# Optimization experiments

Measured on AMD Instinct MI355X. Metric: run time of the kernel, lower is better.

The kernel has to match this reference:

```python
import jax, jax.numpy as jnp
import numpy as np

DIM = 192
HEADS = 6
HSP = 8
WSP = 8
POS_DIM = (DIM // 4) // 4  # 12


def _ln(x, g, b, eps=1e-5):
    m = jnp.mean(x, -1, keepdims=True)
    v = jnp.mean((x - m) ** 2, -1, keepdims=True)
    return (x - m) / jnp.sqrt(v + eps) * g + b


def _rel_tables():
    # rpe_biases: ((2*HSP-1)*(2*WSP-1), 2) float coords of all relative offsets
    bh, bw = np.meshgrid(np.arange(1 - HSP, HSP), np.arange(1 - WSP, WSP), indexing='ij')
    biases = np.stack([bh, bw], -1).reshape(-1, 2).astype(np.float32)
    # relative_position_index: (N, N) int lookup into the bias table
    ch, cw = np.meshgrid(np.arange(HSP), np.arange(WSP), indexing='ij')
    coords = np.stack([ch, cw], 0).reshape(2, -1)  # (2, N)
    rel = coords[:, :, None] - coords[:, None, :]  # (2, N, N)
    idx = (rel[0] + HSP - 1) * (2 * WSP - 1) + (rel[1] + WSP - 1)
    return jnp.asarray(biases), jnp.asarray(idx.astype(np.int32))


def setup_inputs() -> dict:
    key = jax.random.key(0)
    ks = jax.random.split(key, 8)
    B, H, W = 2, 256, 256
    L = H * W
    def lin(k, i, o):
        return jax.random.normal(k, (i, o), jnp.float32) * 0.02
    return {
        'qkv': jax.random.normal(ks[0], (3, B, L, DIM), jnp.float32),
        'w_proj': lin(ks[1], 2, POS_DIM), 'b_proj': jnp.zeros((POS_DIM,), jnp.float32),
        'g1': jnp.ones((POS_DIM,), jnp.float32), 'be1': jnp.zeros((POS_DIM,), jnp.float32),
        'w1': lin(ks[2], POS_DIM, POS_DIM), 'b1': jnp.zeros((POS_DIM,), jnp.float32),
        'g2': jnp.ones((POS_DIM,), jnp.float32), 'be2': jnp.zeros((POS_DIM,), jnp.float32),
        'w2': lin(ks[3], POS_DIM, POS_DIM), 'b2': jnp.zeros((POS_DIM,), jnp.float32),
        'g3': jnp.ones((POS_DIM,), jnp.float32), 'be3': jnp.zeros((POS_DIM,), jnp.float32),
        'w3': lin(ks[4], POS_DIM, HEADS), 'b3': jnp.zeros((HEADS,), jnp.float32),
        'H': H, 'W': W,
    }


def reference(qkv, w_proj, b_proj, g1, be1, w1, b1, g2, be2, w2, b2, g3, be3, w3, b3, H, W):
    B, L, C = qkv.shape[1], qkv.shape[2], qkv.shape[3]
    hd = C // HEADS
    scale = float(hd) ** -0.5
    N = HSP * WSP

    def im2win(x):
        # (B, L, C) -> (B*nW, heads, N, hd)
        x = x.reshape(B, H // HSP, HSP, W // WSP, WSP, C)
        x = x.transpose(0, 1, 3, 2, 4, 5).reshape(-1, N, HEADS, hd)
        return x.transpose(0, 2, 1, 3)

    q = im2win(qkv[0]) * scale
    k = im2win(qkv[1])
    v = im2win(qkv[2])

    attn = jnp.einsum('whnd,whmd->whnm', q, k)  # (B*nW, heads, N, N)

    # dynamic relative position bias via MLP (DynamicPosBias, residual=False)
    biases, rel_idx = _rel_tables()
    p = biases @ w_proj + b_proj
    p = jax.nn.relu(_ln(p, g1, be1)) @ w1 + b1
    p = jax.nn.relu(_ln(p, g2, be2)) @ w2 + b2
    p = jax.nn.relu(_ln(p, g3, be3)) @ w3 + b3  # (n_rel, heads)
    rpb = p[rel_idx.reshape(-1)].reshape(N, N, HEADS).transpose(2, 0, 1)  # (heads, N, N)
    attn = attn + rpb[None]

    attn = jax.nn.softmax(attn, axis=-1)
    x = jnp.einsum('whnm,whmd->whnd', attn, v)  # (B*nW, heads, N, hd)
    x = x.transpose(0, 2, 1, 3).reshape(-1, N, C)

    # windows2img: (B*nW, N, C) -> (B, H, W, C)
    x = x.reshape(B, H // HSP, W // WSP, HSP, WSP, C)
    x = x.transpose(0, 1, 3, 2, 4, 5).reshape(B, H, W, C)
    return x
```

## Files before the change

### kernel.cpp

```cpp
#include <hip/hip_runtime.h>
#include <hip/hip_bf16.h>

#define NHEADS 6
#define HD 32
#define CDIM 192
#define NTOK 64
#define NREL 225
#define PDIM 12
#define IMG 256
#define NWIN 2048
#define SCALE 0.17677669529663687f
#define INV_SCALE 5.656854249492381f

typedef __attribute__((ext_vector_type(8))) short v8s;
typedef __attribute__((ext_vector_type(4))) float v4f;

#define KS2 200
#define VTS 72
#define PTS 72

__device__ __forceinline__ unsigned pkbf(float x, float y) {
    __hip_bfloat162 h = __float22bfloat162_rn(make_float2(x, y));
    union { __hip_bfloat162 h; unsigned u; } c; c.h = h;
    return c.u;
}

__device__ __forceinline__ void ln_relu12(const float* x, const float* g,
                                          const float* be, float* y) {
    float m = 0.f;
#pragma unroll
    for (int i = 0; i < PDIM; ++i) m += x[i];
    m *= (1.f / PDIM);
    float v = 0.f;
#pragma unroll
    for (int i = 0; i < PDIM; ++i) { float d = x[i] - m; v += d * d; }
    v *= (1.f / PDIM);
    float inv = rsqrtf(v + 1e-5f);
#pragma unroll
    for (int i = 0; i < PDIM; ++i) {
        float t = (x[i] - m) * inv * g[i] + be[i];
        y[i] = t > 0.f ? t : 0.f;
    }
}

__global__ __launch_bounds__(512) void win_attn_fused(
    const float* __restrict__ qkv,
    const float* __restrict__ wp, const float* __restrict__ bp,
    const float* __restrict__ g1, const float* __restrict__ be1,
    const float* __restrict__ w1, const float* __restrict__ b1,
    const float* __restrict__ g2, const float* __restrict__ be2,
    const float* __restrict__ w2, const float* __restrict__ b2,
    const float* __restrict__ g3, const float* __restrict__ be3,
    const float* __restrict__ w3, const float* __restrict__ b3,
    float* __restrict__ out)
{
    __shared__ __align__(16) unsigned short ks[NTOK * KS2];
    __shared__ __align__(16) unsigned short vt[CDIM * VTS];
    __shared__ __align__(16) unsigned short pt[2][NTOK * PTS];
    __shared__ float psh[NHEADS * NREL];

    const int t = threadIdx.x;
    const int win = blockIdx.x;
    const int b  = win >> 10;
    const int bh = (win >> 5) & 31;
    const int bw = win & 31;

    const int lane = t & 63;
    const int wave = t >> 6;
    const int rg   = wave & 3;
    const int hh   = wave >> 2;
    const int hbase = hh * 3;
    const int lw = lane & 15;
    const int lg = lane >> 4;
    const int rowbase = rg * 16;

    const size_t PL = (size_t)2 * IMG * IMG * CDIM;
    const float* qplane = qkv + (size_t)b * IMG * IMG * CDIM;
    const float* kplane = qplane + PL;
    const float* vplane = kplane + PL;

    auto pixoff = [&](int tok) -> size_t {
        return ((size_t)(bh * 8 + (tok >> 3)) * IMG + (bw * 8 + (tok & 7))) * CDIM;
    };

#pragma unroll
    for (int pass = 0; pass < 6; ++pass) {
        int fidx = t + pass * 512;
        int s   = fidx / 384;
        int rem = fidx - s * 384;
        int j1  = rem / 48;
        int f   = rem - j1 * 48;
        float4 k4 = *(const float4*)(kplane
                     + ((size_t)(bh * 8 + s) * IMG + (bw * 8 + j1)) * CDIM + f * 4);
        uint2 kk; kk.x = pkbf(k4.x, k4.y); kk.y = pkbf(k4.z, k4.w);
        *(uint2*)&ks[(s * 8 + j1) * KS2 + f * 4] = kk;
    }

    {
        const int u  = t & 31;
        const int dg = (t >> 5) & 7;
        const int vh = t >> 8;
        const int ta = (u & 15) + (u >> 4) * 32;
        const int db = dg * 4;
        const int kpa = (u & 15) * 4 + (u >> 4) * 2;
        const size_t offa = pixoff(ta), offb = pixoff(ta + 16);
#pragma unroll
        for (int hi = 0; hi < 3; ++hi) {
            int h = vh * 3 + hi;
            float4 va = *(const float4*)(vplane + offa + h * HD + db);
            float4 vb = *(const float4*)(vplane + offb + h * HD + db);
            int row = h * HD + db;
            *(unsigned*)&vt[(row + 0) * VTS + kpa] = pkbf(va.x, vb.x);
            *(unsigned*)&vt[(row + 1) * VTS + kpa] = pkbf(va.y, vb.y);
            *(unsigned*)&vt[(row + 2) * VTS + kpa] = pkbf(va.z, vb.z);
            *(unsigned*)&vt[(row + 3) * VTS + kpa] = pkbf(va.w, vb.w);
        }
    }

    v8s aq[3];
    {
        const size_t qoff = pixoff(rowbase + lw);
#pragma unroll
        for (int hi = 0; hi < 3; ++hi) {
            const float* qp = qplane + qoff + (hbase + hi) * HD + lg * 8;
            float4 q0 = *(const float4*)qp;
            float4 q1 = *(const float4*)(qp + 4);
            union { v8s v; unsigned x[4]; } au;
            au.x[0] = pkbf(q0.x, q0.y);
            au.x[1] = pkbf(q0.z, q0.w);
            au.x[2] = pkbf(q1.x, q1.y);
            au.x[3] = pkbf(q1.z, q1.w);
            aq[hi] = au.v;
        }
    }

    if (t < NREL) {
        float x0 = (float)(t / 15 - 7);
        float x1 = (float)(t % 15 - 7);
        float h[PDIM], y[PDIM];
#pragma unroll
        for (int o = 0; o < PDIM; ++o)
            h[o] = x0 * wp[o] + x1 * wp[PDIM + o] + bp[o];
        ln_relu12(h, g1, be1, y);
#pragma unroll
        for (int o = 0; o < PDIM; ++o) {
            float a = b1[o];
#pragma unroll
            for (int i = 0; i < PDIM; ++i) a += y[i] * w1[i * PDIM + o];
            h[o] = a;
        }
        ln_relu12(h, g2, be2, y);
#pragma unroll
        for (int o = 0; o < PDIM; ++o) {
            float a = b2[o];
#pragma unroll
            for (int i = 0; i < PDIM; ++i) a += y[i] * w2[i * PDIM + o];
            h[o] = a;
        }
        ln_relu12(h, g3, be3, y);
#pragma unroll
        for (int o = 0; o < NHEADS; ++o) {
            float a = b3[o];
#pragma unroll
            for (int i = 0; i < PDIM; ++i) a += y[i] * w3[i * NHEADS + o];
            psh[o * NREL + t] = a * INV_SCALE;
        }
    }
    __syncthreads();

    int base_r[4];
    size_t ooff[4];
#pragma unroll
    for (int r = 0; r < 4; ++r) {
        int n = rowbase + lg * 4 + r;
        base_r[r] = ((n >> 3) - (lw >> 3) + 7) * 15 + (n & 7) - (lw & 7) + 7;
        ooff[r] = ((size_t)(b * IMG + bh * 8 + (n >> 3)) * IMG
                   + (bw * 8 + (n & 7))) * CDIM;
    }

#pragma unroll
    for (int hi = 0; hi < 3; ++hi) {
        const int h = hbase + hi;
        v4f acc[4];
#pragma unroll
        for (int ct = 0; ct < 4; ++ct) {
            v4f z = {0.f, 0.f, 0.f, 0.f};
            v8s bfr = *(const v8s*)&ks[(ct * 16 + lw) * KS2 + h * HD + lg * 8];
            acc[ct] = __builtin_amdgcn_mfma_f32_16x16x32_bf16(aq[hi], bfr, z, 0, 0, 0);
        }
        const float* ph = &psh[h * NREL];
        v4f s4 = {0.f, 0.f, 0.f, 0.f};
#pragma unroll
        for (int ct = 0; ct < 4; ++ct)
#pragma unroll
            for (int r = 0; r < 4; ++r) {
                float e = __expf((acc[ct][r] + ph[base_r[r] - ct * 30]) * SCALE);
                acc[ct][r] = e;
                s4[r] += e;
            }
#pragma unroll
        for (int off = 1; off < 16; off <<= 1)
#pragma unroll
            for (int r = 0; r < 4; ++r)
                s4[r] += __shfl_xor(s4[r], off);
        v4f rinv;
#pragma unroll
        for (int r = 0; r < 4; ++r) rinv[r] = __builtin_amdgcn_rcpf(s4[r]);
#pragma unroll
        for (int r = 0; r < 4; ++r) {
            uint2 w;
            w.x = pkbf(acc[0][r], acc[1][r]);
            w.y = pkbf(acc[2][r], acc[3][r]);
            *(uint2*)&pt[hh][(rowbase + lg * 4 + r) * PTS + lw * 4] = w;
        }
        v8s pa[2];
#pragma unroll
        for (int kt = 0; kt < 2; ++kt)
            pa[kt] = *(const v8s*)&pt[hh][(rowbase + lw) * PTS + kt * 32 + lg * 8];
        v4f acc2[2] = {};
#pragma unroll
        for (int dt = 0; dt < 2; ++dt)
#pragma unroll
            for (int kt = 0; kt < 2; ++kt) {
                v8s vb = *(const v8s*)&vt[(h * HD + dt * 16 + lw) * VTS
                                          + kt * 32 + lg * 8];
                acc2[dt] = __builtin_amdgcn_mfma_f32_16x16x32_bf16(pa[kt], vb, acc2[dt], 0, 0, 0);
            }
#pragma unroll
        for (int dt = 0; dt < 2; ++dt)
#pragma unroll
            for (int r = 0; r < 4; ++r)
                out[ooff[r] + h * HD + dt * 16 + lw] = acc2[dt][r] * rinv[r];
    }
}

extern "C" void kernel_launch(void* const* d_in, const int* in_sizes, int n_in,
                              void* d_out, int out_size, void* d_ws, size_t ws_size,
                              hipStream_t stream) {
    const float* qkv = (const float*)d_in[0];
    win_attn_fused<<<NWIN, 512, 0, stream>>>(
        qkv,
        (const float*)d_in[1], (const float*)d_in[2],
        (const float*)d_in[3], (const float*)d_in[4],
        (const float*)d_in[5], (const float*)d_in[6],
        (const float*)d_in[7], (const float*)d_in[8],
        (const float*)d_in[9], (const float*)d_in[10],
        (const float*)d_in[11], (const float*)d_in[12],
        (const float*)d_in[13], (const float*)d_in[14],
        (float*)d_out);
}
```

Before: 88.26 us.

## Fold softmax scale into Q, use exp2, compute row sums via MFMA

Pre-multiplies Q by scale*log2e so the softmax uses raw v_exp_f32 with the bias pre-scaled by log2e. The bias table is re-laid out as float4 per relative index, holding three heads and swizzled by wave half, so one LDS load serves all three heads. QK MFMAs for all heads are hoisted ahead of the exps. Row sums now come from an extra MFMA against a ones vector on the bf16 P, replacing the shuffle reductions, and launch bounds add a min-blocks hint. The trade-offs are more live registers and row sums taken from bf16-rounded probabilities, which differ slightly in precision.

```diff
diff --git a/kernel.cpp b/kernel.cpp
--- a/kernel.cpp
+++ b/kernel.cpp
@@ -9,8 +9,8 @@
 #define PDIM 12
 #define IMG 256
 #define NWIN 2048
-#define SCALE 0.17677669529663687f
-#define INV_SCALE 5.656854249492381f
+#define QSCALE 0.2550348686f
+#define LOG2E 1.4426950408889634f
 
 typedef __attribute__((ext_vector_type(8))) short v8s;
 typedef __attribute__((ext_vector_type(4))) float v4f;
@@ -25,6 +25,10 @@
     return c.u;
 }
 
+__device__ __forceinline__ float ex2(float x) {
+    float r; asm("v_exp_f32 %0, %1" : "=v"(r) : "v"(x)); return r;
+}
+
 __device__ __forceinline__ void ln_relu12(const float* x, const float* g,
                                           const float* be, float* y) {
     float m = 0.f;
@@ -43,7 +47,7 @@
     }
 }
 
-__global__ __launch_bounds__(512) void win_attn_fused(
+__global__ __launch_bounds__(512, 4) void win_attn_fused(
     const float* __restrict__ qkv,
     const float* __restrict__ wp, const float* __restrict__ bp,
     const float* __restrict__ g1, const float* __restrict__ be1,
@@ -57,7 +61,7 @@
     __shared__ __align__(16) unsigned short ks[NTOK * KS2];
     __shared__ __align__(16) unsigned short vt[CDIM * VTS];
     __shared__ __align__(16) unsigned short pt[2][NTOK * PTS];
-    __shared__ float psh[NHEADS * NREL];
+    __shared__ __align__(16) float pshf[NREL * 8];
 
     const int t = threadIdx.x;
     const int win = blockIdx.x;
@@ -126,10 +130,10 @@
             float4 q0 = *(const float4*)qp;
             float4 q1 = *(const float4*)(qp + 4);
             union { v8s v; unsigned x[4]; } au;
-            au.x[0] = pkbf(q0.x, q0.y);
-            au.x[1] = pkbf(q0.z, q0.w);
-            au.x[2] = pkbf(q1.x, q1.y);
-            au.x[3] = pkbf(q1.z, q1.w);
+            au.x[0] = pkbf(q0.x * QSCALE, q0.y * QSCALE);
+            au.x[1] = pkbf(q0.z * QSCALE, q0.w * QSCALE);
+            au.x[2] = pkbf(q1.x * QSCALE, q1.y * QSCALE);
+            au.x[3] = pkbf(q1.z * QSCALE, q1.w * QSCALE);
             aq[hi] = au.v;
         }
     }
@@ -158,59 +162,67 @@
             h[o] = a;
         }
         ln_relu12(h, g3, be3, y);
+        const int sw = (t >> 2) & 1;
 #pragma unroll
         for (int o = 0; o < NHEADS; ++o) {
             float a = b3[o];
 #pragma unroll
             for (int i = 0; i < PDIM; ++i) a += y[i] * w3[i * NHEADS + o];
-            psh[o * NREL + t] = a * INV_SCALE;
+            int half = (o >= 3) ? 1 : 0;
+            pshf[(t * 2 + (half ^ sw)) * 4 + (o - half * 3)] = a * LOG2E;
         }
     }
     __syncthreads();
 
     int base_r[4];
-    size_t ooff[4];
 #pragma unroll
     for (int r = 0; r < 4; ++r) {
         int n = rowbase + lg * 4 + r;
         base_r[r] = ((n >> 3) - (lw >> 3) + 7) * 15 + (n & 7) - (lw & 7) + 7;
+    }
+
+    v4f acc[3][4];
+#pragma unroll
+    for (int ct = 0; ct < 4; ++ct) {
+#pragma unroll
+        for (int hi = 0; hi < 3; ++hi) {
+            v4f z = {0.f, 0.f, 0.f, 0.f};
+            v8s bfr = *(const v8s*)&ks[(ct * 16 + lw) * KS2 + (hbase + hi) * HD + lg * 8];
+            acc[hi][ct] = __builtin_amdgcn_mfma_f32_16x16x32_bf16(aq[hi], bfr, z, 0, 0, 0);
+        }
+    }
+
+#pragma unroll
+    for (int ct = 0; ct < 4; ++ct)
+#pragma unroll
+        for (int r = 0; r < 4; ++r) {
+            int idx = base_r[r] - ct * 30;
+            const float4 bb = *(const float4*)&pshf[(idx * 2 + (hh ^ ((idx >> 2) & 1))) * 4];
+            acc[0][ct][r] = ex2(acc[0][ct][r] + bb.x);
+            acc[1][ct][r] = ex2(acc[1][ct][r] + bb.y);
+            acc[2][ct][r] = ex2(acc[2][ct][r] + bb.z);
+        }
+
+    size_t ooff[4];
+#pragma unroll
+    for (int r = 0; r < 4; ++r) {
+        int n = rowbase + lg * 4 + r;
         ooff[r] = ((size_t)(b * IMG + bh * 8 + (n >> 3)) * IMG
                    + (bw * 8 + (n & 7))) * CDIM;
     }
 
+    v8s ones;
+#pragma unroll
+    for (int j = 0; j < 8; ++j) ones[j] = (short)0x3F80;
+
 #pragma unroll
     for (int hi = 0; hi < 3; ++hi) {
         const int h = hbase + hi;
-        v4f acc[4];
-#pragma unroll
-        for (int ct = 0; ct < 4; ++ct) {
-            v4f z = {0.f, 0.f, 0.f, 0.f};
-            v8s bfr = *(const v8s*)&ks[(ct * 16 + lw) * KS2 + h * HD + lg * 8];
-            acc[ct] = __builtin_amdgcn_mfma_f32_16x16x32_bf16(aq[hi], bfr, z, 0, 0, 0);
-        }
-        const float* ph = &psh[h * NREL];
-        v4f s4 = {0.f, 0.f, 0.f, 0.f};
-#pragma unroll
-        for (int ct = 0; ct < 4; ++ct)
-#pragma unroll
-            for (int r = 0; r < 4; ++r) {
-                float e = __expf((acc[ct][r] + ph[base_r[r] - ct * 30]) * SCALE);
-                acc[ct][r] = e;
-                s4[r] += e;
-            }
-#pragma unroll
-        for (int off = 1; off < 16; off <<= 1)
-#pragma unroll
-            for (int r = 0; r < 4; ++r)
-                s4[r] += __shfl_xor(s4[r], off);
-        v4f rinv;
-#pragma unroll
-        for (int r = 0; r < 4; ++r) rinv[r] = __builtin_amdgcn_rcpf(s4[r]);
 #pragma unroll
         for (int r = 0; r < 4; ++r) {
             uint2 w;
-            w.x = pkbf(acc[0][r], acc[1][r]);
-            w.y = pkbf(acc[2][r], acc[3][r]);
+            w.x = pkbf(acc[hi][0][r], acc[hi][1][r]);
+            w.y = pkbf(acc[hi][2][r], acc[hi][3][r]);
             *(uint2*)&pt[hh][(rowbase + lg * 4 + r) * PTS + lw * 4] = w;
         }
         v8s pa[2];
@@ -218,14 +230,20 @@
         for (int kt = 0; kt < 2; ++kt)
             pa[kt] = *(const v8s*)&pt[hh][(rowbase + lw) * PTS + kt * 32 + lg * 8];
         v4f acc2[2] = {};
-#pragma unroll
-        for (int dt = 0; dt < 2; ++dt)
-#pragma unroll
-            for (int kt = 0; kt < 2; ++kt) {
+        v4f acc3 = {0.f, 0.f, 0.f, 0.f};
+#pragma unroll
+        for (int kt = 0; kt < 2; ++kt) {
+#pragma unroll
+            for (int dt = 0; dt < 2; ++dt) {
                 v8s vb = *(const v8s*)&vt[(h * HD + dt * 16 + lw) * VTS
                                           + kt * 32 + lg * 8];
                 acc2[dt] = __builtin_amdgcn_mfma_f32_16x16x32_bf16(pa[kt], vb, acc2[dt], 0, 0, 0);
             }
+            acc3 = __builtin_amdgcn_mfma_f32_16x16x32_bf16(pa[kt], ones, acc3, 0, 0, 0);
+        }
+        v4f rinv;
+#pragma unroll
+        for (int r = 0; r < 4; ++r) rinv[r] = __builtin_amdgcn_rcpf(acc3[r]);
 #pragma unroll
         for (int dt = 0; dt < 2; ++dt)
 #pragma unroll
```

Result: no change. 88.82 us (+0.6%).
